# Performance work log

Measured on AMD Instinct MI355X. Metric: run time of the kernel, lower is better.

## Reference

```python
import jax, jax.numpy as jnp
import numpy as np

D_MODEL = 512
N_STATE = 64
BATCH = 8
SEQ_L = 2048


def setup_inputs() -> dict:
    key = jax.random.key(0)
    k_u, k_cr, k_ci, k_dt = jax.random.split(key, 4)
    u = jax.random.normal(k_u, (BATCH, SEQ_L, D_MODEL), dtype=jnp.float32)
    # S4D-Lin init: A = -0.5 + i*n
    A_re = -0.5 * jnp.ones((D_MODEL, N_STATE), dtype=jnp.float32)
    A_im = jnp.broadcast_to(jnp.arange(N_STATE, dtype=jnp.float32)[None, :], (D_MODEL, N_STATE))
    C_re = jax.random.normal(k_cr, (D_MODEL, N_STATE), dtype=jnp.float32)
    C_im = jax.random.normal(k_ci, (D_MODEL, N_STATE), dtype=jnp.float32)
    log_dt = (jax.random.uniform(k_dt, (D_MODEL,), dtype=jnp.float32)
              * (np.log(0.1) - np.log(0.001)) + np.log(0.001))
    return {"u": u, "A_re": A_re, "A_im": A_im, "C_re": C_re, "C_im": C_im, "log_dt": log_dt}


def reference(u, A_re, A_im, C_re, C_im, log_dt):
    # u: (batch, L, d_model)
    L = u.shape[1]
    A = A_re + 1j * A_im                     # (d, n) complex
    C = C_re + 1j * C_im                     # (d, n) complex
    B = jnp.ones_like(A)                     # (d, n) complex ones
    dt = jnp.exp(log_dt)                     # (d,)
    delta = dt[:, None] * A                  # (d, n)
    A_bar = jnp.exp(delta)                   # (d, n)
    eps = 1e-8
    B_bar = dt[:, None] * B * (jnp.exp(delta) - 1 + eps) / (delta + eps)  # (d, n)
    v = jnp.arange(L)
    A_bar_v = A_bar[:, :, None] ** v         # (d, n, L) Vandermonde powers
    K = jnp.einsum('dn,dnl,dn->dl', C, A_bar_v, B_bar).real  # (d, L)
    # FFT convolution (circular on 2L -> linear conv, keep first L)
    n_fft = 2 * L
    k_f = jnp.fft.rfft(K, n=n_fft)                       # (d, L+1)
    u_f = jnp.fft.rfft(jnp.swapaxes(u, 1, 2), n=n_fft)   # (b, d, L+1)
    y = jnp.fft.irfft(k_f * u_f, n=n_fft)[..., :L]        # (b, d, L)
    return jnp.swapaxes(y, 1, 2)             # (b, L, d)
```

## Files before the change

### kernel.cpp

```cpp
#include <hip/hip_runtime.h>

#define BB 8
#define LL 2048
#define DD 512
#define NN 64
#define TT 64
#define CC 32

typedef __attribute__((ext_vector_type(8))) short bf16x8;
typedef __attribute__((ext_vector_type(4))) float f32x4;

__device__ __forceinline__ float2 cmul(float2 a, float2 b) {
  return make_float2(a.x*b.x - a.y*b.y, a.x*b.y + a.y*b.x);
}
__device__ __forceinline__ unsigned f2b(float f) {
  union { float f; unsigned u; } v; v.f = f;
  return (v.u + 0x7FFFu + ((v.u >> 16) & 1u)) >> 16;
}
__device__ __forceinline__ float b2f(unsigned h) {
  union { unsigned u; float f; } v; v.u = h << 16; return v.f;
}

__global__ __launch_bounds__(256) void k0_tr(
    const float* __restrict__ u, float* __restrict__ ut) {
  int bid = blockIdx.x;
  int dt8 = bid & 7, lt = (bid >> 3) & 31, b = bid >> 8;
  int l0 = lt * 64, d0 = dt8 * 64;
  int tid = threadIdx.x;
  __shared__ float tl[64][65];
  #pragma unroll
  for (int it = 0; it < 2; ++it) {
    int row = it * 32 + (tid >> 3), seg = tid & 7;
    const float* src = &u[((size_t)(b*LL + l0 + row))*DD + d0 + seg*8];
    float4 v0 = *(const float4*)src;
    float4 v1 = *(const float4*)(src + 4);
    tl[row][seg*8+0]=v0.x; tl[row][seg*8+1]=v0.y;
    tl[row][seg*8+2]=v0.z; tl[row][seg*8+3]=v0.w;
    tl[row][seg*8+4]=v1.x; tl[row][seg*8+5]=v1.y;
    tl[row][seg*8+6]=v1.z; tl[row][seg*8+7]=v1.w;
  }
  __syncthreads();
  #pragma unroll
  for (int it = 0; it < 2; ++it) {
    int row = it * 32 + (tid >> 3), seg = tid & 7;
    float o[8];
    #pragma unroll
    for (int j = 0; j < 8; ++j) o[j] = tl[seg*8 + j][row];
    float* dst = &ut[((size_t)(b*DD + d0 + row))*LL + l0 + seg*8];
    *(float4*)dst = *(float4*)&o[0];
    *(float4*)(dst + 4) = *(float4*)&o[4];
  }
}

__global__ __launch_bounds__(256) void k1_setup(
    const float* __restrict__ A_re, const float* __restrict__ A_im,
    const float* __restrict__ C_re, const float* __restrict__ C_im,
    const float* __restrict__ log_dt,
    ushort* __restrict__ W2s, ushort* __restrict__ G2s,
    ushort* __restrict__ Th2s, ushort* __restrict__ Tl2s,
    float2* __restrict__ P) {
  int d = blockIdx.x;
  int tid = threadIdx.x;
  int n = tid & 63, wv = tid >> 6;
  int idx = d * NN + n;

  __shared__ ushort Wl[8192], Gl[8192];
  __shared__ __align__(16) char smU[16640];
  ushort* Thl = (ushort*)smU;
  ushort* Tll = (ushort*)(smU + 8192);
  float*  Kp  = (float*)smU;
  __shared__ float Kq[64][5];
  __shared__ float Kl[64];

  float dt  = expf(log_dt[d]);
  float dre = dt * A_re[idx], dim = dt * A_im[idx];
  float er  = expf(dre);
  float abr = er * cosf(dim), abi = er * sinf(dim);
  const float eps = 1e-8f;
  float nre = abr - 1.0f + eps, nim = abi;
  float qre = dre + eps,        qim = dim;
  float inv = 1.0f / (qre*qre + qim*qim);
  float bbr = dt * (nre*qre + nim*qim) * inv;
  float bbi = dt * (nim*qre - nre*qim) * inv;
  float2 a  = make_float2(abr, abi);
  float2 bb = make_float2(bbr, bbi);
  float2 cc = make_float2(C_re[idx], C_im[idx]);

  float2 a2  = cmul(a, a),   a4  = cmul(a2, a2);
  float2 a8  = cmul(a4, a4), a16 = cmul(a8, a8);
  float2 a32 = cmul(a16, a16), a48 = cmul(a32, a16);
  float2 pw_wv = make_float2(1.f, 0.f);
  for (int q = 0; q < wv; ++q) pw_wv = cmul(pw_wv, a16);

  if (wv == 0) P[idx] = cmul(a32, a32);

  {
    float2 sel = (wv == 0) ? a48 : (wv == 1) ? a32
               : (wv == 2) ? a16 : make_float2(1.f, 0.f);
    float2 w = cmul(bb, sel);
    for (int j = 15; j >= 0; --j) {
      int s = wv*16 + j;
      int ks = s >> 5, lk = (s >> 3) & 3, e = s & 7;
      {
        int n2 = 2*n; int nh = n2>>6, tq = (n2>>4)&3, lr = n2&15;
        Wl[(((nh*4+tq)*2+ks)*64 + lk*16+lr)*8 + e] = (ushort)f2b(w.x);
      }
      {
        int n2 = 2*n+1; int nh = n2>>6, tq = (n2>>4)&3, lr = n2&15;
        Wl[(((nh*4+tq)*2+ks)*64 + lk*16+lr)*8 + e] = (ushort)f2b(w.y);
      }
      w = cmul(w, a);
    }
  }
  {
    float2 g = cmul(cc, cmul(a, pw_wv));
    for (int j = 0; j < 16; ++j) {
      int r = wv*16 + j;
      int rh = r >> 5, tq = (r >> 4) & 1, lr = r & 15;
      {
        int n2 = 2*n; int ks = n2>>5, lk = (n2>>3)&3, e = n2&7;
        Gl[(((rh*2+tq)*4+ks)*64 + lk*16+lr)*8 + e] = (ushort)f2b(g.x);
      }
      {
        int n2 = 2*n+1; int ks = n2>>5, lk = (n2>>3)&3, e = n2&7;
        Gl[(((rh*2+tq)*4+ks)*64 + lk*16+lr)*8 + e] = (ushort)f2b(-g.y);
      }
      g = cmul(g, a);
    }
  }
  {
    float2 cb = cmul(cc, bb);
    float2 t = cmul(cb, pw_wv);
    for (int j = 0; j < 16; ++j) {
      Kp[(wv*16 + j)*65 + n] = t.x;
      t = cmul(t, a);
    }
  }
  __syncthreads();
  {
    int m = tid >> 2, q = tid & 3;
    float s = 0.f;
    #pragma unroll
    for (int j = 0; j < 16; ++j) s += Kp[m*65 + q*16 + j];
    Kq[m][q] = s;
  }
  __syncthreads();
  if (tid < 64) Kl[tid] = Kq[tid][0] + Kq[tid][1] + Kq[tid][2] + Kq[tid][3];
  __syncthreads();

  {
    int tq = wv >> 1, ks = wv & 1;
    #pragma unroll
    for (int rh = 0; rh < 2; ++rh) {
      int r = rh*32 + tq*16 + (n & 15);
      #pragma unroll
      for (int e = 0; e < 8; ++e) {
        int s = ks*32 + (n >> 4)*8 + e;
        float val = (s <= r) ? Kl[r - s] : 0.f;
        unsigned hv = f2b(val);
        int o = rh*2048 + (wv*64 + n)*8 + e;
        Thl[o] = (ushort)hv;
        Tll[o] = (ushort)f2b(val - b2f(hv));
      }
    }
  }
  __syncthreads();
  {
    uint4* Wg  = (uint4*)(W2s  + (size_t)d * 8192);
    uint4* Gg  = (uint4*)(G2s  + (size_t)d * 8192);
    uint4* Thg = (uint4*)(Th2s + (size_t)d * 4096);
    uint4* Tlg = (uint4*)(Tl2s + (size_t)d * 4096);
    #pragma unroll
    for (int i = tid; i < 1024; i += 256) {
      Wg[i] = ((const uint4*)Wl)[i];
      Gg[i] = ((const uint4*)Gl)[i];
    }
    #pragma unroll
    for (int i = tid; i < 512; i += 256) {
      Thg[i] = ((const uint4*)Thl)[i];
      Tlg[i] = ((const uint4*)Tll)[i];
    }
  }
}

__global__ __launch_bounds__(256, 4) void k2_mfma(
    const float* __restrict__ ut, const ushort* __restrict__ W2s,
    const ushort* __restrict__ G2s, const ushort* __restrict__ Th2s,
    const ushort* __restrict__ Tl2s, const float2* __restrict__ P,
    float* __restrict__ yt) {
  int bid = blockIdx.x;
  int x = bid & 7;
  int d = x * 64 + ((bid >> 3) & 63);
  int b = bid >> 9;
  int tid = threadIdx.x;
  int l = tid & 63, wv = tid >> 6;
  int lr = l & 15, lk = l >> 4;
  int m0 = (wv & 1) * 16;
  int half = wv >> 1;

  __shared__ __align__(16) char smem[8448 + 8448 + 17160];
  char*  u_hi = smem;
  char*  u_lo = smem + 4224;
  char*  Zs   = smem + 8448;
  float* Sf   = (float*)(smem + 16896);
  char*  ylds = smem;

  {
    const float* up = &ut[((size_t)(b * DD + d)) * LL + tid * 8];
    float4 v0 = *(const float4*)up;
    float4 v1 = *(const float4*)(up + 4);
    float f[8] = {v0.x,v0.y,v0.z,v0.w,v1.x,v1.y,v1.z,v1.w};
    unsigned h[8], lo[8];
    #pragma unroll
    for (int j = 0; j < 8; ++j) {
      h[j]  = f2b(f[j]);
      lo[j] = f2b(f[j] - b2f(h[j]));
    }
    uint4 ph = make_uint4(h[0]|(h[1]<<16), h[2]|(h[3]<<16),
                          h[4]|(h[5]<<16), h[6]|(h[7]<<16));
    uint4 pl = make_uint4(lo[0]|(lo[1]<<16), lo[2]|(lo[3]<<16),
                          lo[4]|(lo[5]<<16), lo[6]|(lo[7]<<16));
    int row = (tid >> 3) + 1;
    int off = row*128 + (((tid & 7) * 16) ^ ((row & 7) << 4));
    *(uint4*)(u_hi + off) = ph;
    *(uint4*)(u_lo + off) = pl;
  }
  if (tid < 8) {
    *(uint4*)(u_hi + tid * 16) = make_uint4(0,0,0,0);
    *(uint4*)(u_lo + tid * 16) = make_uint4(0,0,0,0);
  }
  for (int i = tid; i < 130; i += 256) Sf[i] = 0.f;
  __syncthreads();

  {
    const ushort* Wd = W2s + (size_t)d * 8192 + (size_t)half * 4096;
    f32x4 acc[4] = {{0,0,0,0},{0,0,0,0},{0,0,0,0},{0,0,0,0}};
    #pragma unroll
    for (int ks = 0; ks < 2; ++ks) {
      int arow = m0 + lr + 1;
      bf16x8 af = *(const bf16x8*)(u_hi + arow*128 +
                     ((ks*64 + lk*16) ^ ((arow & 7) << 4)));
      #pragma unroll
      for (int t = 0; t < 4; ++t) {
        bf16x8 bfr = *(const bf16x8*)(Wd + ((t*2 + ks)*64 + l)*8);
        acc[t] = __builtin_amdgcn_mfma_f32_16x16x32_bf16(af, bfr, acc[t], 0,0,0);
      }
    }
    #pragma unroll
    for (int t = 0; t < 4; ++t)
      #pragma unroll
      for (int j = 0; j < 4; ++j) {
        int c  = m0 + lk*4 + j;
        int n2 = half*64 + t*16 + lr;
        int col = (n2 >> 1) + (n2 & 1) * 64;
        Sf[(c + 1) * 130 + col] = acc[t][j];
      }
  }

  f32x4 acc2[2] = {{0,0,0,0},{0,0,0,0}};
  {
    const ushort* Tdh = Th2s + (size_t)d * 4096 + (size_t)half * 2048;
    const ushort* Tdl = Tl2s + (size_t)d * 4096 + (size_t)half * 2048;
    #pragma unroll
    for (int ks = 0; ks < 2; ++ks) {
      int arow = m0 + lr + 1;
      int aoff = (ks*64 + lk*16) ^ ((arow & 7) << 4);
      bf16x8 ah = *(const bf16x8*)(u_hi + arow*128 + aoff);
      bf16x8 al = *(const bf16x8*)(u_lo + arow*128 + aoff);
      #pragma unroll
      for (int t = 0; t < 2; ++t) {
        bf16x8 bh = *(const bf16x8*)(Tdh + ((t*2 + ks)*64 + l)*8);
        bf16x8 bl = *(const bf16x8*)(Tdl + ((t*2 + ks)*64 + l)*8);
        acc2[t] = __builtin_amdgcn_mfma_f32_16x16x32_bf16(ah, bh, acc2[t], 0,0,0);
        acc2[t] = __builtin_amdgcn_mfma_f32_16x16x32_bf16(al, bh, acc2[t], 0,0,0);
        acc2[t] = __builtin_amdgcn_mfma_f32_16x16x32_bf16(ah, bl, acc2[t], 0,0,0);
      }
    }
  }
  __syncthreads();

  {
    int n = tid & 63;
    int rb = 1 + (tid >> 6);
    float2 p = P[(size_t)d * NN + n];
    float vre[8], vim[8];
    #pragma unroll
    for (int q = 0; q < 8; ++q) {
      int r = rb + 4*q;
      vre[q] = Sf[r*130 + n];
      vim[q] = Sf[r*130 + 64 + n];
    }
    #pragma unroll
    for (int k = 0; k < 5; ++k) {
      int s = 1 << k;
      float pre[8], pim[8];
      #pragma unroll
      for (int q = 0; q < 8; ++q) {
        int pr = rb + 4*q - s; if (pr < 0) pr = 0;
        pre[q] = Sf[pr*130 + n];
        pim[q] = Sf[pr*130 + 64 + n];
      }
      __syncthreads();
      #pragma unroll
      for (int q = 0; q < 8; ++q) {
        vre[q] = fmaf(p.x, pre[q], fmaf(-p.y, pim[q], vre[q]));
        vim[q] = fmaf(p.x, pim[q], fmaf( p.y, pre[q], vim[q]));
        Sf[(rb + 4*q)*130 + n]      = vre[q];
        Sf[(rb + 4*q)*130 + 64 + n] = vim[q];
      }
      float npx = p.x*p.x - p.y*p.y;
      p.y = 2.f * p.x * p.y; p.x = npx;
      __syncthreads();
    }
    #pragma unroll
    for (int q = 0; q < 8; ++q) {
      int r = rb + 4*q;
      unsigned pk = f2b(vre[q]) | (f2b(vim[q]) << 16);
      *(unsigned*)(Zs + r*256 + ((4*n) ^ ((r & 7) << 4))) = pk;
    }
    if (tid < 64) *(unsigned*)(Zs + 4*tid) = 0u;
  }
  __syncthreads();

  {
    const ushort* Gd = G2s + (size_t)d * 8192 + (size_t)half * 4096;
    #pragma unroll
    for (int ks = 0; ks < 4; ++ks) {
      int arow = m0 + lr;
      bf16x8 af = *(const bf16x8*)(Zs + arow*256 +
                     ((ks*64 + lk*16) ^ ((arow & 7) << 4)));
      #pragma unroll
      for (int t = 0; t < 2; ++t) {
        bf16x8 bfr = *(const bf16x8*)(Gd + ((t*4 + ks)*64 + l)*8);
        acc2[t] = __builtin_amdgcn_mfma_f32_16x16x32_bf16(af, bfr, acc2[t], 0,0,0);
      }
    }
  }
  #pragma unroll
  for (int t = 0; t < 2; ++t)
    #pragma unroll
    for (int j = 0; j < 4; ++j) {
      int c = m0 + lk*4 + j;
      int r = half*32 + t*16 + lr;
      *(float*)(ylds + (c*64 + r)*4) = acc2[t][j];
    }
  __syncthreads();
  {
    float4 o0 = *(const float4*)(ylds + tid * 32);
    float4 o1 = *(const float4*)(ylds + tid * 32 + 16);
    float* dst = &yt[((size_t)(b * DD + d)) * LL + tid * 8];
    *(float4*)dst = o0;
    *(float4*)(dst + 4) = o1;
  }
}

__global__ __launch_bounds__(256) void k4_tr(
    const float* __restrict__ yt, float* __restrict__ y) {
  int bid = blockIdx.x;
  int dt8 = bid & 7, lt = (bid >> 3) & 31, b = bid >> 8;
  int l0 = lt * 64, d0 = dt8 * 64;
  int tid = threadIdx.x;
  __shared__ float tl[64][65];
  #pragma unroll
  for (int it = 0; it < 2; ++it) {
    int row = it * 32 + (tid >> 3), seg = tid & 7;
    const float* src = &yt[((size_t)(b*DD + d0 + row))*LL + l0 + seg*8];
    float4 v0 = *(const float4*)src;
    float4 v1 = *(const float4*)(src + 4);
    tl[row][seg*8+0]=v0.x; tl[row][seg*8+1]=v0.y;
    tl[row][seg*8+2]=v0.z; tl[row][seg*8+3]=v0.w;
    tl[row][seg*8+4]=v1.x; tl[row][seg*8+5]=v1.y;
    tl[row][seg*8+6]=v1.z; tl[row][seg*8+7]=v1.w;
  }
  __syncthreads();
  #pragma unroll
  for (int it = 0; it < 2; ++it) {
    int row = it * 32 + (tid >> 3), seg = tid & 7;
    float o[8];
    #pragma unroll
    for (int j = 0; j < 8; ++j) o[j] = tl[seg*8 + j][row];
    float* dst = &y[((size_t)(b*LL + l0 + row))*DD + d0 + seg*8];
    *(float4*)dst = *(float4*)&o[0];
    *(float4*)(dst + 4) = *(float4*)&o[4];
  }
}

extern "C" void kernel_launch(void* const* d_in, const int* in_sizes, int n_in,
                              void* d_out, int out_size, void* d_ws, size_t ws_size,
                              hipStream_t stream) {
  const float* u      = (const float*)d_in[0];
  const float* A_re   = (const float*)d_in[1];
  const float* A_im   = (const float*)d_in[2];
  const float* C_re   = (const float*)d_in[3];
  const float* C_im   = (const float*)d_in[4];
  const float* log_dt = (const float*)d_in[5];
  float* y = (float*)d_out;

  float*  yt  = (float*)d_ws;
  float*  ut  = yt + (size_t)BB * DD * LL;
  ushort* W2s = (ushort*)(ut + (size_t)BB * DD * LL);
  ushort* G2s = W2s + (size_t)DD * 8192;
  ushort* Th  = G2s + (size_t)DD * 8192;
  ushort* Tl  = Th  + (size_t)DD * 4096;
  float2* P   = (float2*)(Tl + (size_t)DD * 4096);

  k0_tr   <<<BB * 32 * 8, 256, 0, stream>>>(u, ut);
  k1_setup<<<DD,          256, 0, stream>>>(A_re, A_im, C_re, C_im, log_dt,
                                            W2s, G2s, Th, Tl, P);
  k2_mfma <<<BB * DD,     256, 0, stream>>>(ut, W2s, G2s, Th, Tl, P, yt);
  k4_tr   <<<BB * 32 * 8, 256, 0, stream>>>(yt, y);
}
```

Baseline: 71.33 us.

## Replace log-step chunk scan with serial-plus-carry scan; move bf16 split into transpose

```diff
diff --git a/kernel.cpp b/kernel.cpp
--- a/kernel.cpp
+++ b/kernel.cpp
@@ -22,7 +22,8 @@
 }
 
 __global__ __launch_bounds__(256) void k0_tr(
-    const float* __restrict__ u, float* __restrict__ ut) {
+    const float* __restrict__ u, ushort* __restrict__ uth,
+    ushort* __restrict__ utl) {
   int bid = blockIdx.x;
   int dt8 = bid & 7, lt = (bid >> 3) & 31, b = bid >> 8;
   int l0 = lt * 64, d0 = dt8 * 64;
@@ -43,12 +44,20 @@
   #pragma unroll
   for (int it = 0; it < 2; ++it) {
     int row = it * 32 + (tid >> 3), seg = tid & 7;
-    float o[8];
-    #pragma unroll
-    for (int j = 0; j < 8; ++j) o[j] = tl[seg*8 + j][row];
-    float* dst = &ut[((size_t)(b*DD + d0 + row))*LL + l0 + seg*8];
-    *(float4*)dst = *(float4*)&o[0];
-    *(float4*)(dst + 4) = *(float4*)&o[4];
+    unsigned h[8], lo[8];
+    #pragma unroll
+    for (int j = 0; j < 8; ++j) {
+      float f = tl[seg*8 + j][row];
+      h[j]  = f2b(f);
+      lo[j] = f2b(f - b2f(h[j]));
+    }
+    uint4 ph = make_uint4(h[0]|(h[1]<<16), h[2]|(h[3]<<16),
+                          h[4]|(h[5]<<16), h[6]|(h[7]<<16));
+    uint4 pl = make_uint4(lo[0]|(lo[1]<<16), lo[2]|(lo[3]<<16),
+                          lo[4]|(lo[5]<<16), lo[6]|(lo[7]<<16));
+    size_t off = ((size_t)(b*DD + d0 + row))*LL + l0 + seg*8;
+    *(uint4*)&uth[off] = ph;
+    *(uint4*)&utl[off] = pl;
   }
 }
 
@@ -184,10 +193,10 @@
 }
 
 __global__ __launch_bounds__(256, 4) void k2_mfma(
-    const float* __restrict__ ut, const ushort* __restrict__ W2s,
-    const ushort* __restrict__ G2s, const ushort* __restrict__ Th2s,
-    const ushort* __restrict__ Tl2s, const float2* __restrict__ P,
-    float* __restrict__ yt) {
+    const ushort* __restrict__ uth, const ushort* __restrict__ utl,
+    const ushort* __restrict__ W2s, const ushort* __restrict__ G2s,
+    const ushort* __restrict__ Th2s, const ushort* __restrict__ Tl2s,
+    const float2* __restrict__ P, float* __restrict__ yt) {
   int bid = blockIdx.x;
   int x = bid & 7;
   int d = x * 64 + ((bid >> 3) & 63);
@@ -198,38 +207,23 @@
   int m0 = (wv & 1) * 16;
   int half = wv >> 1;
 
-  __shared__ __align__(16) char smem[8448 + 8448 + 17160];
+  __shared__ __align__(16) char smem[8448 + 8192 + 17160];
   char*  u_hi = smem;
   char*  u_lo = smem + 4224;
   char*  Zs   = smem + 8448;
-  float* Sf   = (float*)(smem + 16896);
+  float* Sf   = (float*)(smem + 16640);
+  __shared__ float2 Tb[4][64];
   char*  ylds = smem;
 
   {
-    const float* up = &ut[((size_t)(b * DD + d)) * LL + tid * 8];
-    float4 v0 = *(const float4*)up;
-    float4 v1 = *(const float4*)(up + 4);
-    float f[8] = {v0.x,v0.y,v0.z,v0.w,v1.x,v1.y,v1.z,v1.w};
-    unsigned h[8], lo[8];
-    #pragma unroll
-    for (int j = 0; j < 8; ++j) {
-      h[j]  = f2b(f[j]);
-      lo[j] = f2b(f[j] - b2f(h[j]));
-    }
-    uint4 ph = make_uint4(h[0]|(h[1]<<16), h[2]|(h[3]<<16),
-                          h[4]|(h[5]<<16), h[6]|(h[7]<<16));
-    uint4 pl = make_uint4(lo[0]|(lo[1]<<16), lo[2]|(lo[3]<<16),
-                          lo[4]|(lo[5]<<16), lo[6]|(lo[7]<<16));
+    size_t off = ((size_t)(b * DD + d)) * LL + tid * 8;
+    uint4 vh = *(const uint4*)&uth[off];
+    uint4 vl = *(const uint4*)&utl[off];
     int row = (tid >> 3) + 1;
-    int off = row*128 + (((tid & 7) * 16) ^ ((row & 7) << 4));
-    *(uint4*)(u_hi + off) = ph;
-    *(uint4*)(u_lo + off) = pl;
-  }
-  if (tid < 8) {
-    *(uint4*)(u_hi + tid * 16) = make_uint4(0,0,0,0);
-    *(uint4*)(u_lo + tid * 16) = make_uint4(0,0,0,0);
-  }
-  for (int i = tid; i < 130; i += 256) Sf[i] = 0.f;
+    int bo = row*128 + (((tid & 7) * 16) ^ ((row & 7) << 4));
+    *(uint4*)(u_hi + bo) = vh;
+    *(uint4*)(u_lo + bo) = vl;
+  }
   __syncthreads();
 
   {
@@ -281,44 +275,37 @@
 
   {
     int n = tid & 63;
-    int rb = 1 + (tid >> 6);
     float2 p = P[(size_t)d * NN + n];
-    float vre[8], vim[8];
-    #pragma unroll
-    for (int q = 0; q < 8; ++q) {
-      int r = rb + 4*q;
-      vre[q] = Sf[r*130 + n];
-      vim[q] = Sf[r*130 + 64 + n];
-    }
-    #pragma unroll
-    for (int k = 0; k < 5; ++k) {
-      int s = 1 << k;
-      float pre[8], pim[8];
-      #pragma unroll
-      for (int q = 0; q < 8; ++q) {
-        int pr = rb + 4*q - s; if (pr < 0) pr = 0;
-        pre[q] = Sf[pr*130 + n];
-        pim[q] = Sf[pr*130 + 64 + n];
-      }
-      __syncthreads();
-      #pragma unroll
-      for (int q = 0; q < 8; ++q) {
-        vre[q] = fmaf(p.x, pre[q], fmaf(-p.y, pim[q], vre[q]));
-        vim[q] = fmaf(p.x, pim[q], fmaf( p.y, pre[q], vim[q]));
-        Sf[(rb + 4*q)*130 + n]      = vre[q];
-        Sf[(rb + 4*q)*130 + 64 + n] = vim[q];
-      }
-      float npx = p.x*p.x - p.y*p.y;
-      p.y = 2.f * p.x * p.y; p.x = npx;
-      __syncthreads();
-    }
-    #pragma unroll
-    for (int q = 0; q < 8; ++q) {
-      int r = rb + 4*q;
-      unsigned pk = f2b(vre[q]) | (f2b(vim[q]) << 16);
-      *(unsigned*)(Zs + r*256 + ((4*n) ^ ((r & 7) << 4))) = pk;
-    }
-    if (tid < 64) *(unsigned*)(Zs + 4*tid) = 0u;
+    float2 z[8], loc[8];
+    #pragma unroll
+    for (int j = 0; j < 8; ++j) {
+      int r = wv*8 + j + 1;
+      z[j].x = Sf[r*130 + n];
+      z[j].y = Sf[r*130 + 64 + n];
+    }
+    loc[0] = z[0];
+    #pragma unroll
+    for (int j = 1; j < 8; ++j)
+      loc[j] = make_float2(fmaf(p.x, loc[j-1].x, fmaf(-p.y, loc[j-1].y, z[j].x)),
+                           fmaf(p.x, loc[j-1].y, fmaf( p.y, loc[j-1].x, z[j].y)));
+    Tb[wv][n] = loc[7];
+    float2 p2 = cmul(p, p), p4 = cmul(p2, p2), p8 = cmul(p4, p4);
+    __syncthreads();
+    float2 Cw = make_float2(0.f, 0.f);
+    for (int ww = 0; ww < wv; ++ww) {
+      float2 t = Tb[ww][n];
+      Cw = make_float2(fmaf(p8.x, Cw.x, fmaf(-p8.y, Cw.y, t.x)),
+                       fmaf(p8.x, Cw.y, fmaf( p8.y, Cw.x, t.y)));
+    }
+    float2 q = Cw;
+    *(unsigned*)(Zs + (wv*8)*256 + (4*n)) = f2b(q.x) | (f2b(q.y) << 16);
+    #pragma unroll
+    for (int j = 1; j < 8; ++j) {
+      q = cmul(p, q);
+      float2 v = make_float2(loc[j-1].x + q.x, loc[j-1].y + q.y);
+      *(unsigned*)(Zs + (wv*8 + j)*256 + ((4*n) ^ (j << 4))) =
+          f2b(v.x) | (f2b(v.y) << 16);
+    }
   }
   __syncthreads();
 
@@ -342,12 +329,13 @@
     for (int j = 0; j < 4; ++j) {
       int c = m0 + lk*4 + j;
       int r = half*32 + t*16 + lr;
-      *(float*)(ylds + (c*64 + r)*4) = acc2[t][j];
-    }
-  __syncthreads();
-  {
-    float4 o0 = *(const float4*)(ylds + tid * 32);
-    float4 o1 = *(const float4*)(ylds + tid * 32 + 16);
+      *(float*)(ylds + (c*68 + r)*4) = acc2[t][j];
+    }
+  __syncthreads();
+  {
+    int row = tid >> 3, col = (tid & 7) * 8;
+    float4 o0 = *(const float4*)(ylds + (row*68 + col)*4);
+    float4 o1 = *(const float4*)(ylds + (row*68 + col + 4)*4);
     float* dst = &yt[((size_t)(b * DD + d)) * LL + tid * 8];
     *(float4*)dst = o0;
     *(float4*)(dst + 4) = o1;
@@ -397,16 +385,17 @@
   float* y = (float*)d_out;
 
   float*  yt  = (float*)d_ws;
-  float*  ut  = yt + (size_t)BB * DD * LL;
-  ushort* W2s = (ushort*)(ut + (size_t)BB * DD * LL);
+  ushort* uth = (ushort*)(yt + (size_t)BB * DD * LL);
+  ushort* utl = uth + (size_t)BB * DD * LL;
+  ushort* W2s = utl + (size_t)BB * DD * LL;
   ushort* G2s = W2s + (size_t)DD * 8192;
   ushort* Th  = G2s + (size_t)DD * 8192;
   ushort* Tl  = Th  + (size_t)DD * 4096;
   float2* P   = (float2*)(Tl + (size_t)DD * 4096);
 
-  k0_tr   <<<BB * 32 * 8, 256, 0, stream>>>(u, ut);
+  k0_tr   <<<BB * 32 * 8, 256, 0, stream>>>(u, uth, utl);
   k1_setup<<<DD,          256, 0, stream>>>(A_re, A_im, C_re, C_im, log_dt,
                                             W2s, G2s, Th, Tl, P);
-  k2_mfma <<<BB * DD,     256, 0, stream>>>(ut, W2s, G2s, Th, Tl, P, yt);
+  k2_mfma <<<BB * DD,     256, 0, stream>>>(uth, utl, W2s, G2s, Th, Tl, P, yt);
   k4_tr   <<<BB * 32 * 8, 256, 0, stream>>>(yt, y);
 }
```

Measured after the change: 65.80 us. 7.8% less time.

## Split u to bf16 hi/lo in transpose, add lo-term MFMAs, preload weights to registers

Applied to the files above, without the earlier changes.

```diff
diff --git a/kernel.cpp b/kernel.cpp
--- a/kernel.cpp
+++ b/kernel.cpp
@@ -22,7 +22,8 @@
 }
 
 __global__ __launch_bounds__(256) void k0_tr(
-    const float* __restrict__ u, float* __restrict__ ut) {
+    const float* __restrict__ u, ushort* __restrict__ uth,
+    ushort* __restrict__ utl) {
   int bid = blockIdx.x;
   int dt8 = bid & 7, lt = (bid >> 3) & 31, b = bid >> 8;
   int l0 = lt * 64, d0 = dt8 * 64;
@@ -43,12 +44,20 @@
   #pragma unroll
   for (int it = 0; it < 2; ++it) {
     int row = it * 32 + (tid >> 3), seg = tid & 7;
-    float o[8];
-    #pragma unroll
-    for (int j = 0; j < 8; ++j) o[j] = tl[seg*8 + j][row];
-    float* dst = &ut[((size_t)(b*DD + d0 + row))*LL + l0 + seg*8];
-    *(float4*)dst = *(float4*)&o[0];
-    *(float4*)(dst + 4) = *(float4*)&o[4];
+    unsigned h[8], lo[8];
+    #pragma unroll
+    for (int j = 0; j < 8; ++j) {
+      float f = tl[seg*8 + j][row];
+      h[j]  = f2b(f);
+      lo[j] = f2b(f - b2f(h[j]));
+    }
+    uint4 ph = make_uint4(h[0]|(h[1]<<16), h[2]|(h[3]<<16),
+                          h[4]|(h[5]<<16), h[6]|(h[7]<<16));
+    uint4 pl = make_uint4(lo[0]|(lo[1]<<16), lo[2]|(lo[3]<<16),
+                          lo[4]|(lo[5]<<16), lo[6]|(lo[7]<<16));
+    size_t off = ((size_t)(b*DD + d0 + row))*LL + l0 + seg*8;
+    *(uint4*)&uth[off] = ph;
+    *(uint4*)&utl[off] = pl;
   }
 }
 
@@ -183,11 +192,11 @@
   }
 }
 
-__global__ __launch_bounds__(256, 4) void k2_mfma(
-    const float* __restrict__ ut, const ushort* __restrict__ W2s,
-    const ushort* __restrict__ G2s, const ushort* __restrict__ Th2s,
-    const ushort* __restrict__ Tl2s, const float2* __restrict__ P,
-    float* __restrict__ yt) {
+__global__ __launch_bounds__(256, 3) void k2_mfma(
+    const ushort* __restrict__ uth, const ushort* __restrict__ utl,
+    const ushort* __restrict__ W2s, const ushort* __restrict__ G2s,
+    const ushort* __restrict__ Th2s, const ushort* __restrict__ Tl2s,
+    const float2* __restrict__ P, float* __restrict__ yt) {
   int bid = blockIdx.x;
   int x = bid & 7;
   int d = x * 64 + ((bid >> 3) & 63);
@@ -198,52 +207,58 @@
   int m0 = (wv & 1) * 16;
   int half = wv >> 1;
 
-  __shared__ __align__(16) char smem[8448 + 8448 + 17160];
+  __shared__ __align__(16) char smem[50960];
   char*  u_hi = smem;
-  char*  u_lo = smem + 4224;
-  char*  Zs   = smem + 8448;
-  float* Sf   = (float*)(smem + 16896);
-  char*  ylds = smem;
-
-  {
-    const float* up = &ut[((size_t)(b * DD + d)) * LL + tid * 8];
-    float4 v0 = *(const float4*)up;
-    float4 v1 = *(const float4*)(up + 4);
-    float f[8] = {v0.x,v0.y,v0.z,v0.w,v1.x,v1.y,v1.z,v1.w};
-    unsigned h[8], lo[8];
-    #pragma unroll
-    for (int j = 0; j < 8; ++j) {
-      h[j]  = f2b(f[j]);
-      lo[j] = f2b(f[j] - b2f(h[j]));
-    }
-    uint4 ph = make_uint4(h[0]|(h[1]<<16), h[2]|(h[3]<<16),
-                          h[4]|(h[5]<<16), h[6]|(h[7]<<16));
-    uint4 pl = make_uint4(lo[0]|(lo[1]<<16), lo[2]|(lo[3]<<16),
-                          lo[4]|(lo[5]<<16), lo[6]|(lo[7]<<16));
-    int row = (tid >> 3) + 1;
-    int off = row*128 + (((tid & 7) * 16) ^ ((row & 7) << 4));
-    *(uint4*)(u_hi + off) = ph;
-    *(uint4*)(u_lo + off) = pl;
-  }
-  if (tid < 8) {
-    *(uint4*)(u_hi + tid * 16) = make_uint4(0,0,0,0);
-    *(uint4*)(u_lo + tid * 16) = make_uint4(0,0,0,0);
+  char*  u_lo = smem + 4096;
+  float* Sf   = (float*)(smem + 8192);
+  char*  Zs   = smem + 25360;
+  char*  Zl   = smem + 33808;
+  float* ylds = (float*)(smem + 42256);
+
+  bf16x8 wf[8], tfh[4], tfl[4];
+  {
+    const ushort* Wd  = W2s  + (size_t)d * 8192 + (size_t)half * 4096;
+    const ushort* Tdh = Th2s + (size_t)d * 4096 + (size_t)half * 2048;
+    const ushort* Tdl = Tl2s + (size_t)d * 4096 + (size_t)half * 2048;
+    #pragma unroll
+    for (int t = 0; t < 4; ++t)
+      #pragma unroll
+      for (int ks = 0; ks < 2; ++ks)
+        wf[t*2+ks] = *(const bf16x8*)(Wd + ((t*2 + ks)*64 + l)*8);
+    #pragma unroll
+    for (int t = 0; t < 2; ++t)
+      #pragma unroll
+      for (int ks = 0; ks < 2; ++ks) {
+        tfh[t*2+ks] = *(const bf16x8*)(Tdh + ((t*2 + ks)*64 + l)*8);
+        tfl[t*2+ks] = *(const bf16x8*)(Tdl + ((t*2 + ks)*64 + l)*8);
+      }
+  }
+  float2 p0 = P[(size_t)d * NN + l];
+
+  {
+    size_t off = ((size_t)(b * DD + d)) * LL + tid * 8;
+    uint4 vh = *(const uint4*)&uth[off];
+    uint4 vl = *(const uint4*)&utl[off];
+    int row = tid >> 3;
+    int bo = row*128 + (((tid & 7) * 16) ^ ((row & 7) << 4));
+    *(uint4*)(u_hi + bo) = vh;
+    *(uint4*)(u_lo + bo) = vl;
   }
   for (int i = tid; i < 130; i += 256) Sf[i] = 0.f;
   __syncthreads();
 
   {
-    const ushort* Wd = W2s + (size_t)d * 8192 + (size_t)half * 4096;
     f32x4 acc[4] = {{0,0,0,0},{0,0,0,0},{0,0,0,0},{0,0,0,0}};
     #pragma unroll
     for (int ks = 0; ks < 2; ++ks) {
-      int arow = m0 + lr + 1;
-      bf16x8 af = *(const bf16x8*)(u_hi + arow*128 +
-                     ((ks*64 + lk*16) ^ ((arow & 7) << 4)));
+      int arow = m0 + lr;
+      int aoff = (ks*64 + lk*16) ^ ((arow & 7) << 4);
+      bf16x8 ah = *(const bf16x8*)(u_hi + arow*128 + aoff);
+      bf16x8 al = *(const bf16x8*)(u_lo + arow*128 + aoff);
       #pragma unroll
       for (int t = 0; t < 4; ++t) {
-        bf16x8 bfr = *(const bf16x8*)(Wd + ((t*2 + ks)*64 + l)*8);
-        acc[t] = __builtin_amdgcn_mfma_f32_16x16x32_bf16(af, bfr, acc[t], 0,0,0);
+        acc[t] = __builtin_amdgcn_mfma_f32_16x16x32_bf16(ah, wf[t*2+ks], acc[t], 0,0,0);
+        acc[t] = __builtin_amdgcn_mfma_f32_16x16x32_bf16(al, wf[t*2+ks], acc[t], 0,0,0);
       }
     }
     #pragma unroll
@@ -259,30 +274,36 @@
 
   f32x4 acc2[2] = {{0,0,0,0},{0,0,0,0}};
   {
-    const ushort* Tdh = Th2s + (size_t)d * 4096 + (size_t)half * 2048;
-    const ushort* Tdl = Tl2s + (size_t)d * 4096 + (size_t)half * 2048;
     #pragma unroll
     for (int ks = 0; ks < 2; ++ks) {
-      int arow = m0 + lr + 1;
+      int arow = m0 + lr;
       int aoff = (ks*64 + lk*16) ^ ((arow & 7) << 4);
       bf16x8 ah = *(const bf16x8*)(u_hi + arow*128 + aoff);
       bf16x8 al = *(const bf16x8*)(u_lo + arow*128 + aoff);
       #pragma unroll
       for (int t = 0; t < 2; ++t) {
-        bf16x8 bh = *(const bf16x8*)(Tdh + ((t*2 + ks)*64 + l)*8);
-        bf16x8 bl = *(const bf16x8*)(Tdl + ((t*2 + ks)*64 + l)*8);
-        acc2[t] = __builtin_amdgcn_mfma_f32_16x16x32_bf16(ah, bh, acc2[t], 0,0,0);
-        acc2[t] = __builtin_amdgcn_mfma_f32_16x16x32_bf16(al, bh, acc2[t], 0,0,0);
-        acc2[t] = __builtin_amdgcn_mfma_f32_16x16x32_bf16(ah, bl, acc2[t], 0,0,0);
-      }
-    }
+        acc2[t] = __builtin_amdgcn_mfma_f32_16x16x32_bf16(ah, tfh[t*2+ks], acc2[t], 0,0,0);
+        acc2[t] = __builtin_amdgcn_mfma_f32_16x16x32_bf16(al, tfh[t*2+ks], acc2[t], 0,0,0);
+        acc2[t] = __builtin_amdgcn_mfma_f32_16x16x32_bf16(ah, tfl[t*2+ks], acc2[t], 0,0,0);
+      }
+    }
+  }
+
+  bf16x8 gf[8];
+  {
+    const ushort* Gd = G2s + (size_t)d * 8192 + (size_t)half * 4096;
+    #pragma unroll
+    for (int t = 0; t < 2; ++t)
+      #pragma unroll
+      for (int ks = 0; ks < 4; ++ks)
+        gf[t*4+ks] = *(const bf16x8*)(Gd + ((t*4 + ks)*64 + l)*8);
   }
   __syncthreads();
 
   {
     int n = tid & 63;
     int rb = 1 + (tid >> 6);
-    float2 p = P[(size_t)d * NN + n];
+    float2 p = p0;
     float vre[8], vim[8];
     #pragma unroll
     for (int q = 0; q < 8; ++q) {
@@ -315,39 +336,48 @@
     #pragma unroll
     for (int q = 0; q < 8; ++q) {
       int r = rb + 4*q;
-      unsigned pk = f2b(vre[q]) | (f2b(vim[q]) << 16);
-      *(unsigned*)(Zs + r*256 + ((4*n) ^ ((r & 7) << 4))) = pk;
-    }
-    if (tid < 64) *(unsigned*)(Zs + 4*tid) = 0u;
-  }
-  __syncthreads();
-
-  {
-    const ushort* Gd = G2s + (size_t)d * 8192 + (size_t)half * 4096;
+      unsigned hx = f2b(vre[q]), hy = f2b(vim[q]);
+      unsigned lx = f2b(vre[q] - b2f(hx)), ly = f2b(vim[q] - b2f(hy));
+      int off = r*256 + ((4*n) ^ ((r & 7) << 4));
+      *(unsigned*)(Zs + off) = hx | (hy << 16);
+      *(unsigned*)(Zl + off) = lx | (ly << 16);
+    }
+    if (tid < 64) {
+      *(unsigned*)(Zs + 4*tid) = 0u;
+      *(unsigned*)(Zl + 4*tid) = 0u;
+    }
+  }
+  __syncthreads();
+
+  {
     #pragma unroll
     for (int ks = 0; ks < 4; ++ks) {
       int arow = m0 + lr;
-      bf16x8 af = *(const bf16x8*)(Zs + arow*256 +
-                     ((ks*64 + lk*16) ^ ((arow & 7) << 4)));
+      int aoff = (ks*64 + lk*16) ^ ((arow & 7) << 4);
+      bf16x8 ah = *(const bf16x8*)(Zs + arow*256 + aoff);
+      bf16x8 al = *(const bf16x8*)(Zl + arow*256 + aoff);
       #pragma unroll
       for (int t = 0; t < 2; ++t) {
-        bf16x8 bfr = *(const bf16x8*)(Gd + ((t*4 + ks)*64 + l)*8);
-        acc2[t] = __builtin_amdgcn_mfma_f32_16x16x32_bf16(af, bfr, acc2[t], 0,0,0);
-      }
-    }
-  }
+        acc2[t] = __builtin_amdgcn_mfma_f32_16x16x32_bf16(ah, gf[t*4+ks], acc2[t], 0,0,0);
+        acc2[t] = __builtin_amdgcn_mfma_f32_16x16x32_bf16(al, gf[t*4+ks], acc2[t], 0,0,0);
+      }
+    }
+  }
+  __syncthreads();
+
   #pragma unroll
   for (int t = 0; t < 2; ++t)
     #pragma unroll
     for (int j = 0; j < 4; ++j) {
       int c = m0 + lk*4 + j;
       int r = half*32 + t*16 + lr;
-      *(float*)(ylds + (c*64 + r)*4) = acc2[t][j];
-    }
-  __syncthreads();
-  {
-    float4 o0 = *(const float4*)(ylds + tid * 32);
-    float4 o1 = *(const float4*)(ylds + tid * 32 + 16);
+      ylds[c*68 + r] = acc2[t][j];
+    }
+  __syncthreads();
+  {
+    int row = tid >> 3, col = (tid & 7) * 8;
+    float4 o0 = *(const float4*)&ylds[row*68 + col];
+    float4 o1 = *(const float4*)&ylds[row*68 + col + 4];
     float* dst = &yt[((size_t)(b * DD + d)) * LL + tid * 8];
     *(float4*)dst = o0;
     *(float4*)(dst + 4) = o1;
@@ -397,16 +427,17 @@
   float* y = (float*)d_out;
 
   float*  yt  = (float*)d_ws;
-  float*  ut  = yt + (size_t)BB * DD * LL;
-  ushort* W2s = (ushort*)(ut + (size_t)BB * DD * LL);
+  ushort* uth = (ushort*)(yt + (size_t)BB * DD * LL);
+  ushort* utl = uth + (size_t)BB * DD * LL;
+  ushort* W2s = utl + (size_t)BB * DD * LL;
   ushort* G2s = W2s + (size_t)DD * 8192;
   ushort* Th  = G2s + (size_t)DD * 8192;
   ushort* Tl  = Th  + (size_t)DD * 4096;
   float2* P   = (float2*)(Tl + (size_t)DD * 4096);
 
-  k0_tr   <<<BB * 32 * 8, 256, 0, stream>>>(u, ut);
+  k0_tr   <<<BB * 32 * 8, 256, 0, stream>>>(u, uth, utl);
   k1_setup<<<DD,          256, 0, stream>>>(A_re, A_im, C_re, C_im, log_dt,
                                             W2s, G2s, Th, Tl, P);
-  k2_mfma <<<BB * DD,     256, 0, stream>>>(ut, W2s, G2s, Th, Tl, P, yt);
+  k2_mfma <<<BB * DD,     256, 0, stream>>>(uth, utl, W2s, G2s, Th, Tl, P, yt);
   k4_tr   <<<BB * 32 * 8, 256, 0, stream>>>(yt, y);
 }
```

Result: slower. 72.92 us (+2.2%).
